# Kernel optimization log

Measured on AMD Instinct MI355X. Metric: run time of the kernel, lower is better.

Reference implementation:

```python
import jax, jax.numpy as jnp
import numpy as np

STEP = 1.0  # module init arg
N = 8192


def setup_inputs() -> dict:
    key = jax.random.key(0)
    k1, = jax.random.split(key, 1)
    predictions = jax.random.normal(k1, (N, 1), dtype=jnp.float32) * 50.0  # depth-like values
    z_spacing = jnp.ones((), dtype=jnp.float32) * 2.5
    nth_slice = jnp.ones((), dtype=jnp.float32) * 4.0
    return {"predictions": predictions, "z_spacing": z_spacing, "nth_slice": nth_slice}


def reference(predictions, z_spacing, nth_slice):
    p = predictions[:, 0]                       # [N]
    n = p.shape[0]
    acceptable_step = STEP * z_spacing * nth_slice
    # closed form of the loop-built step matrix: steps[i,j] = |i-j| * acceptable_step
    idx = jnp.arange(n)
    steps = jnp.abs(idx[:, None] - idx[None, :]).astype(p.dtype) * acceptable_step  # [N,N]
    d = p[:, None] - p[None, :]                 # [N,N] pairwise differences
    # first masked update: where d >= 0, subtract 0.2*steps
    d = jnp.where(d >= 0, d - 0.2 * steps, d)
    # second masked update on the updated d: clamp (d - 0.8*steps) at 0
    d = jnp.where(d >= 0, jnp.maximum(d - 0.8 * steps, jnp.zeros((), d.dtype)), d)
    loss = jnp.sum(jnp.abs(jnp.tril(d))) / (n * n)
    return loss
```

## Files before the change

kernel.cpp:

```cpp
#include <hip/hip_runtime.h>


constexpr int TILE = 256;

__global__ __launch_bounds__(TILE) void depth_loss_kernel(
    const float* __restrict__ p,
    const float* __restrict__ zsp,
    const float* __restrict__ nsl,
    double* __restrict__ partials,
    int n)
{
    int b = blockIdx.x;
    int bi = (int)((sqrtf(8.0f * (float)b + 1.0f) - 1.0f) * 0.5f);
    while ((bi + 1) * (bi + 2) / 2 <= b) ++bi;
    while (bi * (bi + 1) / 2 > b) --bi;
    int bj = b - bi * (bi + 1) / 2;

    int tid = threadIdx.x;
    int i = bi * TILE + tid;
    float pi = (i < n) ? p[i] : 0.0f;

    __shared__ float pj[TILE];
    int jg = bj * TILE + tid;
    pj[tid] = (jg < n) ? p[jg] : 0.0f;
    __syncthreads();

    float a = zsp[0] * nsl[0];
    int jbase = bj * TILE;
    float fi_minus_jbase = (float)(i - jbase);

    float acc = 0.0f;
#pragma unroll 8
    for (int jj = 0; jj < TILE; ++jj) {
        float s  = (fi_minus_jbase - (float)jj) * a;
        float d0 = pi - pj[jj];
        float d1 = d0 - 0.2f * s;
        float d2 = fmaxf(d0 - s, 0.0f);
        float c  = (d0 < 0.0f) ? -d0 : ((d1 < 0.0f) ? -d1 : d2);
        bool valid = (jbase + jj <= i) && (i < n);
        acc += valid ? c : 0.0f;
    }

    for (int off = 32; off > 0; off >>= 1)
        acc += __shfl_down(acc, off, 64);

    __shared__ float wsum[TILE / 64];
    int wave = tid >> 6;
    if ((tid & 63) == 0) wsum[wave] = acc;
    __syncthreads();

    if (tid == 0) {
        float blocksum = 0.0f;
        for (int w = 0; w < TILE / 64; ++w) blocksum += wsum[w];
        partials[b] = (double)blocksum;
    }
}

__global__ __launch_bounds__(256) void finalize_kernel(
    const double* __restrict__ partials, int nblocks, float* __restrict__ out,
    double inv_nn)
{
    int tid = threadIdx.x;
    double acc = 0.0;
    for (int b = tid; b < nblocks; b += 256) acc += partials[b];
    for (int off = 32; off > 0; off >>= 1)
        acc += __shfl_down(acc, off, 64);
    __shared__ double wsum[4];
    if ((tid & 63) == 0) wsum[tid >> 6] = acc;
    __syncthreads();
    if (tid == 0)
        out[0] = (float)((wsum[0] + wsum[1] + wsum[2] + wsum[3]) * inv_nn);
}

extern "C" void kernel_launch(void* const* d_in, const int* in_sizes, int n_in,
                              void* d_out, int out_size, void* d_ws, size_t ws_size,
                              hipStream_t stream) {
    const float* p   = (const float*)d_in[0];
    const float* zsp = (const float*)d_in[1];
    const float* nsl = (const float*)d_in[2];
    float* out = (float*)d_out;
    double* partials = (double*)d_ws;

    int n = in_sizes[0];
    int ntiles = (n + TILE - 1) / TILE;
    int nblocks = ntiles * (ntiles + 1) / 2;
    double inv_nn = 1.0 / ((double)n * (double)n);

    depth_loss_kernel<<<nblocks, TILE, 0, stream>>>(p, zsp, nsl, partials, n);
    finalize_kernel<<<1, 256, 0, stream>>>(partials, nblocks, out, inv_nn);
}
```

Baseline: 75.29 us.

## Split tiles into 256x128 blocks, skip masking off-diagonal, use incremental steps

Column tiles shrink to 128 so the lower triangle is covered by nrt*(nrt+1) blocks, which cuts the work spent on the diagonal. Blocks that lie fully below the diagonal take a branch-free loop with no validity mask. The step value is now updated incrementally instead of recomputed each iteration, and the per-pair logic is reduced to one max-of-two. Shared loads use float4 and the bounds checks on n are gone, so the kernel assumes n is a multiple of 256. Accumulating the step incrementally in float can drift slightly from the exact value.

Measured after the change: 70.59 us. -6.3%, faster.

```diff
diff --git a/kernel.cpp b/kernel.cpp
--- a/kernel.cpp
+++ b/kernel.cpp
@@ -1,58 +1,85 @@
 #include <hip/hip_runtime.h>
 
 
-constexpr int TILE = 256;
+constexpr int ROWS = 256;
+constexpr int COLS = 128;
 
-__global__ __launch_bounds__(TILE) void depth_loss_kernel(
+__global__ __launch_bounds__(ROWS) void depth_loss_kernel(
     const float* __restrict__ p,
     const float* __restrict__ zsp,
     const float* __restrict__ nsl,
-    double* __restrict__ partials,
-    int n)
+    double* __restrict__ partials)
 {
     int b = blockIdx.x;
-    int bi = (int)((sqrtf(8.0f * (float)b + 1.0f) - 1.0f) * 0.5f);
-    while ((bi + 1) * (bi + 2) / 2 <= b) ++bi;
-    while (bi * (bi + 1) / 2 > b) --bi;
-    int bj = b - bi * (bi + 1) / 2;
+    int ri = (int)((sqrtf(4.0f * (float)b + 1.0f) - 1.0f) * 0.5f);
+    while ((ri + 1) * (ri + 2) <= b) ++ri;
+    while (ri * (ri + 1) > b) --ri;
+    int cj = b - ri * (ri + 1);
 
     int tid = threadIdx.x;
-    int i = bi * TILE + tid;
-    float pi = (i < n) ? p[i] : 0.0f;
+    int i = ri * ROWS + tid;
+    float pi = p[i];
 
-    __shared__ float pj[TILE];
-    int jg = bj * TILE + tid;
-    pj[tid] = (jg < n) ? p[jg] : 0.0f;
+    __shared__ __align__(16) float pj[COLS];
+    int jbase = cj * COLS;
+    if (tid < COLS / 4)
+        ((float4*)pj)[tid] = ((const float4*)(p + jbase))[tid];
     __syncthreads();
 
-    float a = zsp[0] * nsl[0];
-    int jbase = bj * TILE;
-    float fi_minus_jbase = (float)(i - jbase);
+    float a   = zsp[0] * nsl[0];
+    float a02 = 0.2f * a;
+    float s   = (float)(i - jbase) * a;
+    float s02 = 0.2f * s;
 
     float acc = 0.0f;
-#pragma unroll 8
-    for (int jj = 0; jj < TILE; ++jj) {
-        float s  = (fi_minus_jbase - (float)jj) * a;
-        float d0 = pi - pj[jj];
-        float d1 = d0 - 0.2f * s;
-        float d2 = fmaxf(d0 - s, 0.0f);
-        float c  = (d0 < 0.0f) ? -d0 : ((d1 < 0.0f) ? -d1 : d2);
-        bool valid = (jbase + jj <= i) && (i < n);
-        acc += valid ? c : 0.0f;
+    const float4* pj4 = (const float4*)pj;
+
+#define PAIR_BODY(PJV, MASKED)                                   \
+    {                                                            \
+        float d0 = pi - (PJV);                                   \
+        float n0 = (PJV) - pi;                                   \
+        float e1 = s02 - d0;                                     \
+        float e2 = d0 - s;                                       \
+        float m  = fmaxf(fmaxf(e1, e2), 0.0f);       \
+        float c  = (d0 < 0.0f) ? n0 : m;                         \
+        if (MASKED) c = (s >= 0.0f) ? c : 0.0f;                  \
+        acc += c;                                                \
+        s   -= a;                                                \
+        s02 -= a02;                                              \
     }
+
+    if (cj < 2 * ri) {
+        #pragma unroll 8
+        for (int q = 0; q < COLS / 4; ++q) {
+            float4 v = pj4[q];
+            PAIR_BODY(v.x, false)
+            PAIR_BODY(v.y, false)
+            PAIR_BODY(v.z, false)
+            PAIR_BODY(v.w, false)
+        }
+    } else {
+        #pragma unroll 8
+        for (int q = 0; q < COLS / 4; ++q) {
+            float4 v = pj4[q];
+            PAIR_BODY(v.x, true)
+            PAIR_BODY(v.y, true)
+            PAIR_BODY(v.z, true)
+            PAIR_BODY(v.w, true)
+        }
+    }
+#undef PAIR_BODY
 
     for (int off = 32; off > 0; off >>= 1)
         acc += __shfl_down(acc, off, 64);
 
-    __shared__ float wsum[TILE / 64];
-    int wave = tid >> 6;
-    if ((tid & 63) == 0) wsum[wave] = acc;
+    __shared__ float wsum[ROWS / 64];
+    if ((tid & 63) == 0) wsum[tid >> 6] = acc;
     __syncthreads();
 
     if (tid == 0) {
         float blocksum = 0.0f;
-        for (int w = 0; w < TILE / 64; ++w) blocksum += wsum[w];
-        partials[b] = (double)blocksum;
+        for (int w = 0; w < ROWS / 64; ++w) blocksum += wsum[w];
+        partials[blockIdx.x] = (double)blocksum;
     }
 }
 
@@ -82,10 +109,10 @@
     double* partials = (double*)d_ws;
 
     int n = in_sizes[0];
-    int ntiles = (n + TILE - 1) / TILE;
-    int nblocks = ntiles * (ntiles + 1) / 2;
+    int nrt = (n + ROWS - 1) / ROWS;
+    int nblocks = nrt * (nrt + 1);
     double inv_nn = 1.0 / ((double)n * (double)n);
 
-    depth_loss_kernel<<<nblocks, TILE, 0, stream>>>(p, zsp, nsl, partials, n);
+    depth_loss_kernel<<<nblocks, ROWS, 0, stream>>>(p, zsp, nsl, partials);
     finalize_kernel<<<1, 256, 0, stream>>>(partials, nblocks, out, inv_nn);
 }
```
